# Performance work log

Hardware: AMD Instinct MI355X
Metric: run time of the kernel (lower is better)

The kernel has to match this reference:

```python
import jax, jax.numpy as jnp
import numpy as np

B, S = 512, 512
VOCAB, E, H1, H2, NTAGS = 50000, 20, 30, 50, 45


def _xavier_scale(fan_in, fan_out):
    return float(np.sqrt(2.0 / (fan_in + fan_out)))


def setup_inputs() -> dict:
    key = jax.random.key(0)
    ks = jax.random.split(key, 32)
    n = lambda i, shape, s=1.0: jax.random.normal(ks[i], shape, dtype=jnp.float32) * s
    w = 0.1  # weight scale
    emb_f1 = n(0, (VOCAB, E), w).at[0].set(0.0)  # padding_idx=0
    emb_b1 = n(1, (VOCAB, E), w).at[0].set(0.0)
    xs1 = _xavier_scale(B, H1)
    xs2 = _xavier_scale(B, H2)
    inp = {
        "x": jax.random.randint(ks[2], (B, S), 0, VOCAB, dtype=jnp.int64),
        "emb_f1": emb_f1, "emb_b1": emb_b1,
        "h0_f1": n(3, (B, H1), xs1), "c0_f1": n(4, (B, H1), xs1),
        "Wih_f1": n(5, (4 * H1, E), w), "Whh_f1": n(6, (4 * H1, H1), w),
        "bih_f1": n(7, (4 * H1,), w), "bhh_f1": n(8, (4 * H1,), w),
        "h0_b1": n(9, (B, H1), xs1), "c0_b1": n(10, (B, H1), xs1),
        "Wih_b1": n(11, (4 * H1, E), w), "Whh_b1": n(12, (4 * H1, H1), w),
        "bih_b1": n(13, (4 * H1,), w), "bhh_b1": n(14, (4 * H1,), w),
        "h0_f2": n(15, (B, H2), xs2), "c0_f2": n(16, (B, H2), xs2),
        "Wih_f2": n(17, (4 * H2, 2 * H1), w), "Whh_f2": n(18, (4 * H2, H2), w),
        "bih_f2": n(19, (4 * H2,), w), "bhh_f2": n(20, (4 * H2,), w),
        "h0_b2": n(21, (B, H2), xs2), "c0_b2": n(22, (B, H2), xs2),
        "Wih_b2": n(23, (4 * H2, 2 * H1), w), "Whh_b2": n(24, (4 * H2, H2), w),
        "bih_b2": n(25, (4 * H2,), w), "bhh_b2": n(26, (4 * H2,), w),
        "lin_w": n(27, (NTAGS, 2 * H2), w), "lin_b": n(28, (NTAGS,), w),
    }
    return inp


def _run_lstm(seq, h0, c0, Wih, Whh, bih, bhh, forward):
    """PyTorch LSTMCell recurrence over seq (B,S,D). Replicates the original's
    quirks: backward dir appends hidden states in reversed time order, and the
    (S,B,H) stack is .view()-ed into (B,S,H) without transposing."""
    b, s, _ = seq.shape
    h = h0.shape[-1]
    xs = jnp.swapaxes(seq, 0, 1)  # (S,B,D)

    def step(carry, xt):
        hh, cc = carry
        g = xt @ Wih.T + bih + hh @ Whh.T + bhh  # (B, 4H), gate order i,f,g,o
        i, f, gg, o = jnp.split(g, 4, axis=-1)
        cc = jax.nn.sigmoid(f) * cc + jax.nn.sigmoid(i) * jnp.tanh(gg)
        hh = jax.nn.sigmoid(o) * jnp.tanh(cc)
        return (hh, cc), hh

    _, hs = jax.lax.scan(step, (h0, c0), xs, reverse=not forward)  # hs[i] ~ time i
    if not forward:
        hs = hs[::-1]  # torch appended in processing (reversed-time) order
    return hs.reshape(b, s, h)  # faithful buggy view (S,B,H) -> (B,S,H)


def reference(x, emb_f1, emb_b1,
              h0_f1, c0_f1, Wih_f1, Whh_f1, bih_f1, bhh_f1,
              h0_b1, c0_b1, Wih_b1, Whh_b1, bih_b1, bhh_b1,
              h0_f2, c0_f2, Wih_f2, Whh_f2, bih_f2, bhh_f2,
              h0_b2, c0_b2, Wih_b2, Whh_b2, bih_b2, bhh_b2,
              lin_w, lin_b):
    f1 = _run_lstm(emb_f1[x], h0_f1, c0_f1, Wih_f1, Whh_f1, bih_f1, bhh_f1, True)
    b1 = _run_lstm(emb_b1[x], h0_b1, c0_b1, Wih_b1, Whh_b1, bih_b1, bhh_b1, False)
    l1 = jnp.concatenate([f1, b1], axis=2)  # (B,S,2*H1)
    f2 = _run_lstm(l1, h0_f2, c0_f2, Wih_f2, Whh_f2, bih_f2, bhh_f2, True)
    b2 = _run_lstm(l1, h0_b2, c0_b2, Wih_b2, Whh_b2, bih_b2, bhh_b2, False)
    l2 = jnp.concatenate([f2, b2], axis=2)  # (B,S,2*H2)
    return l2 @ lin_w.T + lin_b  # (B,S,NTAGS)
```

## Files before the change

### kernel.cpp

```cpp
#include <hip/hip_runtime.h>
#include <hip/hip_bf16.h>

typedef __hip_bfloat16 bf16;
typedef __attribute__((ext_vector_type(8))) short short8;
typedef __attribute__((ext_vector_type(4))) float float4v;
typedef unsigned short ushort_t;

#define BB 512
#define SS 512
#define EE 20
#define H1C 30
#define H2C 50
#define NTC 45

#define BAR() asm volatile("s_waitcnt lgkmcnt(0)\n\ts_barrier" ::: "memory")

#if __has_builtin(__builtin_amdgcn_exp2f)
#define EXP2(x) __builtin_amdgcn_exp2f(x)
#else
#define EXP2(x) exp2f(x)
#endif
#if __has_builtin(__builtin_amdgcn_rcpf)
#define RCPF(x) __builtin_amdgcn_rcpf(x)
#else
#define RCPF(x) (1.0f / (x))
#endif

__device__ __forceinline__ float sigf(float v) {
    return RCPF(1.0f + EXP2(-1.4426950408889634f * v));
}
__device__ __forceinline__ float tanh_(float v) {
    return 2.0f * RCPF(1.0f + EXP2(-2.8853900817779268f * v)) - 1.0f;
}

__device__ __forceinline__ ushort_t f2bf(float f) {
    unsigned u = __float_as_uint(f);
    unsigned r = u + 0x7FFFu + ((u >> 16) & 1u);
    return (ushort_t)(r >> 16);
}
__device__ __forceinline__ float bf2f(ushort_t s) { return __uint_as_float(((unsigned)s) << 16); }

__device__ __forceinline__ float ldG(const void* p, int i, int f32) {
    if (f32) return ((const float*)p)[i];
    return bf2f(((const ushort_t*)p)[i]);
}
__device__ __forceinline__ int ldTok(const void* x, int i, int x64) {
    const int* xi = (const int*)x;
    return x64 ? xi[2 * i] : xi[i];
}

__global__ void detect_kernel(const void* bih, const void* x, int* flags) {
    if (threadIdx.x == 0 && blockIdx.x == 0) {
        const ushort_t* u = (const ushort_t*)bih;
        int isf = 0;
        for (int i = 0; i < 120; i++) {
            float v = fabsf(bf2f(u[i]));
            if (!(v < 16.0f)) isf = 1;
        }
        flags[0] = isf;
        const int* xi = (const int*)x;
        int orv = 0;
        for (int i = 1; i < 32; i += 2) orv |= xi[i];
        flags[1] = (orv == 0) ? 1 : 0;
    }
}

struct XV4 { float v[4]; };

__global__ __launch_bounds__(128) void lstm1_kernel(
    const void* __restrict__ x,
    const void* __restrict__ emb_f, const void* __restrict__ emb_b,
    const void* __restrict__ h0_f, const void* __restrict__ c0_f,
    const void* __restrict__ Wih_f, const void* __restrict__ Whh_f,
    const void* __restrict__ bih_f, const void* __restrict__ bhh_f,
    const void* __restrict__ h0_b, const void* __restrict__ c0_b,
    const void* __restrict__ Wih_b, const void* __restrict__ Whh_b,
    const void* __restrict__ bih_b, const void* __restrict__ bhh_b,
    ushort_t* __restrict__ hsf, ushort_t* __restrict__ hsb,
    const int* __restrict__ flags)
{
    const int f32v = flags[0], x64 = flags[1];
    const int wg = blockIdx.x, dir = wg >> 5, j0 = (wg & 31) << 4, tid = threadIdx.x;
    const int wave = tid >> 6, lane = tid & 63, li = lane & 15, quad = lane >> 4;

    const void* emb = dir ? emb_b : emb_f;
    const void* h0  = dir ? h0_b  : h0_f;
    const void* c0  = dir ? c0_b  : c0_f;
    const void* Wih = dir ? Wih_b : Wih_f;
    const void* Whh = dir ? Whh_b : Whh_f;
    const void* bih = dir ? bih_b : bih_f;
    const void* bhh = dir ? bhh_b : bhh_f;
    ushort_t* hs = dir ? hsb : hsf;

    __shared__ __align__(16) ushort_t Af[2][2][64][8];
    __shared__ int toks[16][SS];

    for (int idx = tid; idx < 16 * SS; idx += 128) {
        int r = idx >> 9, t = idx & (SS - 1);
        toks[r][t] = ldTok(x, (j0 + r) * SS + t, x64);
    }
    for (int idx = tid; idx < 2 * 2 * 64 * 8; idx += 128) ((ushort_t*)Af)[idx] = 0;

    const int n = wave * 16 + li;
    const bool nok = n < H1C;

    short8 bhi[4][2], blo[4][2];
    float bias_g[4];
    #pragma unroll
    for (int g = 0; g < 4; g++) {
        const int wrow = g * H1C + n;
        bias_g[g] = nok ? (ldG(bih, wrow, f32v) + ldG(bhh, wrow, f32v)) : 0.f;
        #pragma unroll
        for (int kt = 0; kt < 2; kt++) {
            short8 hi, lo;
            #pragma unroll
            for (int j = 0; j < 8; j++) {
                int k = kt * 32 + quad * 8 + j;
                float w = 0.f;
                if (nok) {
                    if (k < EE) w = ldG(Wih, wrow * EE + k, f32v);
                    else if (k < EE + H1C) w = ldG(Whh, wrow * H1C + (k - EE), f32v);
                }
                ushort_t h = f2bf(w);
                hi[j] = (short)h;
                lo[j] = (short)f2bf(w - bf2f(h));
            }
            bhi[g][kt] = hi; blo[g][kt] = lo;
        }
    }

    const int kh = EE + n;
    const int khk = kh >> 5, khg = (kh & 31) >> 3, khj = kh & 7;
    const int lrow = tid / 5, lc = tid - lrow * 5, k0 = lc * 4;
    const bool ldr = tid < 80;
    const int t0 = dir ? SS - 1 : 0, dt = dir ? -1 : 1;

    __syncthreads();

    float creg[4];
    #pragma unroll
    for (int r = 0; r < 4; r++) {
        const int m = quad * 4 + r;
        creg[r] = nok ? ldG(c0, (j0 + m) * H1C + n, f32v) : 0.f;
        ushort_t hb = nok ? f2bf(ldG(h0, (j0 + m) * H1C + n, f32v)) : 0;
        Af[0][khk][khg * 16 + m][khj] = hb;
    }
    XV4 xA, xB;
    if (ldr) {
        int tok = toks[lrow][t0];
        #pragma unroll
        for (int jj = 0; jj < 4; jj++)
            Af[0][0][(k0 >> 3) * 16 + lrow][(k0 & 7) + jj] = f2bf(ldG(emb, tok * EE + k0 + jj, f32v));
        int tok1 = toks[lrow][t0 + dt];
        #pragma unroll
        for (int jj = 0; jj < 4; jj++) xA.v[jj] = ldG(emb, tok1 * EE + k0 + jj, f32v);
    }
    __syncthreads();

    auto step = [&](int it, XV4& xin, XV4& xout) {
        const int t = t0 + dt * it;
        const int cur = it & 1, nxt = cur ^ 1;
        BAR();
        short8 af0 = *(const short8*)&Af[cur][0][lane][0];
        short8 af1 = *(const short8*)&Af[cur][1][lane][0];
        if (ldr && it + 2 < SS) {
            int tok = toks[lrow][t + 2 * dt];
            #pragma unroll
            for (int jj = 0; jj < 4; jj++) xout.v[jj] = ldG(emb, tok * EE + k0 + jj, f32v);
        }
        float4v acc[4];
        #pragma unroll
        for (int g = 0; g < 4; g++) {
            float4v a; a[0] = a[1] = a[2] = a[3] = bias_g[g];
            a = __builtin_amdgcn_mfma_f32_16x16x32_bf16(af0, bhi[g][0], a, 0, 0, 0);
            a = __builtin_amdgcn_mfma_f32_16x16x32_bf16(af0, blo[g][0], a, 0, 0, 0);
            a = __builtin_amdgcn_mfma_f32_16x16x32_bf16(af1, bhi[g][1], a, 0, 0, 0);
            a = __builtin_amdgcn_mfma_f32_16x16x32_bf16(af1, blo[g][1], a, 0, 0, 0);
            acc[g] = a;
        }
        ushort_t hb[4];
        #pragma unroll
        for (int r = 0; r < 4; r++) {
            float gi = acc[0][r], gf = acc[1][r], gg = acc[2][r], go = acc[3][r];
            float c = sigf(gf) * creg[r] + sigf(gi) * tanh_(gg);
            float h = sigf(go) * tanh_(c);
            creg[r] = c;
            hb[r] = nok ? f2bf(h) : 0;
            hs[((size_t)(j0 + quad * 4 + r) * SS + t) * 32 + n] = hb[r];
        }
        if (it + 1 < SS) {
            #pragma unroll
            for (int r = 0; r < 4; r++) Af[nxt][khk][khg * 16 + quad * 4 + r][khj] = hb[r];
            if (ldr) {
                #pragma unroll
                for (int jj = 0; jj < 4; jj++)
                    Af[nxt][0][(k0 >> 3) * 16 + lrow][(k0 & 7) + jj] = f2bf(xin.v[jj]);
            }
        }
    };
    for (int it = 0; it < SS; it += 2) { step(it, xA, xB); step(it + 1, xB, xA); }
}

__global__ __launch_bounds__(256) void lstm2_kernel(
    const ushort_t* __restrict__ hs1f, const ushort_t* __restrict__ hs1b,
    const void* __restrict__ h0_f, const void* __restrict__ c0_f,
    const void* __restrict__ Wih_f, const void* __restrict__ Whh_f,
    const void* __restrict__ bih_f, const void* __restrict__ bhh_f,
    const void* __restrict__ h0_b, const void* __restrict__ c0_b,
    const void* __restrict__ Wih_b, const void* __restrict__ Whh_b,
    const void* __restrict__ bih_b, const void* __restrict__ bhh_b,
    ushort_t* __restrict__ hsf, ushort_t* __restrict__ hsb,
    const int* __restrict__ flags)
{
    const int f32v = flags[0];
    const int wg = blockIdx.x, dir = wg >> 5, cb = (wg & 31) << 4, tid = threadIdx.x;
    const int wave = tid >> 6, lane = tid & 63, li = lane & 15, quad = lane >> 4;

    const void* h0  = dir ? h0_b  : h0_f;
    const void* c0  = dir ? c0_b  : c0_f;
    const void* Wih = dir ? Wih_b : Wih_f;
    const void* Whh = dir ? Whh_b : Whh_f;
    const void* bih = dir ? bih_b : bih_f;
    const void* bhh = dir ? bhh_b : bhh_f;
    ushort_t* hs = dir ? hsb : hsf;

    __shared__ __align__(16) ushort_t Af[2][4][64][8];
    for (int idx = tid; idx < 2 * 4 * 64 * 8; idx += 256) ((ushort_t*)Af)[idx] = 0;

    const int n = wave * 16 + li;
    const bool nok = n < H2C;

    short8 bhi[4][4], blo[4][4];
    float bias_g[4];
    #pragma unroll
    for (int g = 0; g < 4; g++) {
        const int wrow = g * H2C + n;
        bias_g[g] = nok ? (ldG(bih, wrow, f32v) + ldG(bhh, wrow, f32v)) : 0.f;
        #pragma unroll
        for (int kt = 0; kt < 4; kt++) {
            short8 hi, lo;
            #pragma unroll
            for (int j = 0; j < 8; j++) {
                int k = kt * 32 + quad * 8 + j;
                float w = 0.f;
                if (nok) {
                    if (k < H1C) w = ldG(Wih, wrow * (2 * H1C) + k, f32v);
                    else if (k >= 32 && k < 32 + H1C) w = ldG(Wih, wrow * (2 * H1C) + H1C + (k - 32), f32v);
                    else if (k >= 64 && k < 64 + H2C) w = ldG(Whh, wrow * H2C + (k - 64), f32v);
                }
                ushort_t h = f2bf(w);
                hi[j] = (short)h;
                lo[j] = (short)f2bf(w - bf2f(h));
            }
            bhi[g][kt] = hi; blo[g][kt] = lo;
        }
    }

    const int kh = 64 + n;
    const int khk = kh >> 5, khg = (kh & 31) >> 3, khj = kh & 7;
    const int lrow = tid >> 4, k0 = (tid & 15) * 4;
    const int t0 = dir ? SS - 1 : 0, dt = dir ? -1 : 1;

    auto loadX = [&](int c) -> ushort4 {
        const int a = cb + lrow;
        if (k0 < 32)
            return *(const ushort4*)&hs1f[((size_t)c * SS + a) * 32 + k0];
        else
            return *(const ushort4*)&hs1b[((size_t)c * SS + (SS - 1 - a)) * 32 + (k0 - 32)];
    };

    __syncthreads();

    float creg[4];
    #pragma unroll
    for (int r = 0; r < 4; r++) {
        const int m = quad * 4 + r;
        creg[r] = nok ? ldG(c0, (cb + m) * H2C + n, f32v) : 0.f;
        ushort_t hb = nok ? f2bf(ldG(h0, (cb + m) * H2C + n, f32v)) : 0;
        Af[0][khk][khg * 16 + m][khj] = hb;
    }
    {
        ushort4 xi = loadX(t0);
        const int kg = (k0 & 31) >> 3, kt = k0 >> 5, jb = k0 & 7;
        Af[0][kt][kg * 16 + lrow][jb + 0] = xi.x;
        Af[0][kt][kg * 16 + lrow][jb + 1] = xi.y;
        Af[0][kt][kg * 16 + lrow][jb + 2] = xi.z;
        Af[0][kt][kg * 16 + lrow][jb + 3] = xi.w;
    }
    ushort4 xA = loadX(t0 + dt), xB;
    __syncthreads();

    auto step = [&](int it, ushort4& xin, ushort4& xout) {
        const int c = t0 + dt * it;
        const int cur = it & 1, nxt = cur ^ 1;
        BAR();
        short8 af[4];
        #pragma unroll
        for (int kt = 0; kt < 4; kt++) af[kt] = *(const short8*)&Af[cur][kt][lane][0];
        if (it + 2 < SS) xout = loadX(c + 2 * dt);
        float4v acc[4];
        #pragma unroll
        for (int g = 0; g < 4; g++) {
            float4v a; a[0] = a[1] = a[2] = a[3] = bias_g[g];
            #pragma unroll
            for (int kt = 0; kt < 4; kt++) {
                a = __builtin_amdgcn_mfma_f32_16x16x32_bf16(af[kt], bhi[g][kt], a, 0, 0, 0);
                a = __builtin_amdgcn_mfma_f32_16x16x32_bf16(af[kt], blo[g][kt], a, 0, 0, 0);
            }
            acc[g] = a;
        }
        ushort_t hb[4];
        #pragma unroll
        for (int r = 0; r < 4; r++) {
            float gi = acc[0][r], gf = acc[1][r], gg = acc[2][r], go = acc[3][r];
            float cc = sigf(gf) * creg[r] + sigf(gi) * tanh_(gg);
            float h = sigf(go) * tanh_(cc);
            creg[r] = cc;
            hb[r] = nok ? f2bf(h) : 0;
        }
        ushort4 h4; h4.x = hb[0]; h4.y = hb[1]; h4.z = hb[2]; h4.w = hb[3];
        *(ushort4*)&hs[((size_t)c * 64 + n) * SS + cb + quad * 4] = h4;
        if (it + 1 < SS) {
            #pragma unroll
            for (int r = 0; r < 4; r++) Af[nxt][khk][khg * 16 + quad * 4 + r][khj] = hb[r];
            const int kg = (k0 & 31) >> 3, kt = k0 >> 5, jb = k0 & 7;
            Af[nxt][kt][kg * 16 + lrow][jb + 0] = xin.x;
            Af[nxt][kt][kg * 16 + lrow][jb + 1] = xin.y;
            Af[nxt][kt][kg * 16 + lrow][jb + 2] = xin.z;
            Af[nxt][kt][kg * 16 + lrow][jb + 3] = xin.w;
        }
    };
    for (int it = 0; it < SS; it += 2) { step(it, xA, xB); step(it + 1, xB, xA); }
}

__global__ __launch_bounds__(256) void lin_kernel(
    const ushort_t* __restrict__ hs2f, const ushort_t* __restrict__ hs2b,
    const void* __restrict__ lw, const void* __restrict__ lb,
    void* __restrict__ out, const int* __restrict__ flags)
{
    const int f32v = flags[0];
    const int tid = threadIdx.x, wave = tid >> 6, lane = tid & 63, li = lane & 15, quad = lane >> 4;

    __shared__ __align__(16) ushort_t Af[4][4][64][8];
    for (int idx = tid; idx < 4 * 4 * 64 * 8; idx += 256) ((ushort_t*)Af)[idx] = 0;

    short8 bhi[3][4], blo[3][4];
    float biasv[3];
    #pragma unroll
    for (int nt = 0; nt < 3; nt++) {
        const int nn = nt * 16 + li;
        const bool nok = nn < NTC;
        biasv[nt] = nok ? ldG(lb, nn, f32v) : 0.f;
        #pragma unroll
        for (int kt = 0; kt < 4; kt++) {
            short8 hi, lo;
            #pragma unroll
            for (int j = 0; j < 8; j++) {
                int k = kt * 32 + quad * 8 + j;
                float w = 0.f;
                if (nok) {
                    if (k < H2C) w = ldG(lw, nn * 100 + k, f32v);
                    else if (k >= 64 && k < 64 + H2C) w = ldG(lw, nn * 100 + 50 + (k - 64), f32v);
                }
                ushort_t h = f2bf(w);
                hi[j] = (short)h;
                lo[j] = (short)f2bf(w - bf2f(h));
            }
            bhi[nt][kt] = hi; blo[nt][kt] = lo;
        }
    }

    const int P0 = blockIdx.x * 64;
    const int i = P0 >> 9, j0 = P0 & 511;
    __syncthreads();
    for (int idx = tid; idx < 100 * 32; idx += 256) {
        const int kk = idx >> 5, pj = (idx & 31) * 2;
        unsigned v;
        int k;
        if (kk < H2C) {
            v = *(const unsigned*)&hs2f[((size_t)i * 64 + kk) * SS + j0 + pj];
            k = kk;
        } else {
            v = *(const unsigned*)&hs2b[((size_t)(SS - 1 - i) * 64 + (kk - H2C)) * SS + j0 + pj];
            k = 64 + (kk - H2C);
        }
        const int kt = k >> 5, kg = (k & 31) >> 3, j = k & 7;
        Af[pj >> 4][kt][kg * 16 + (pj & 15)][j] = (ushort_t)(v & 0xFFFF);
        Af[pj >> 4][kt][kg * 16 + ((pj + 1) & 15)][j] = (ushort_t)(v >> 16);
    }
    __syncthreads();

    short8 af[4];
    #pragma unroll
    for (int kt = 0; kt < 4; kt++) af[kt] = *(const short8*)&Af[wave][kt][lane][0];
    #pragma unroll
    for (int nt = 0; nt < 3; nt++) {
        float4v a; a[0] = a[1] = a[2] = a[3] = biasv[nt];
        #pragma unroll
        for (int kt = 0; kt < 4; kt++) {
            a = __builtin_amdgcn_mfma_f32_16x16x32_bf16(af[kt], bhi[nt][kt], a, 0, 0, 0);
            a = __builtin_amdgcn_mfma_f32_16x16x32_bf16(af[kt], blo[nt][kt], a, 0, 0, 0);
        }
        const int nn = nt * 16 + li;
        if (nn < NTC) {
            #pragma unroll
            for (int reg = 0; reg < 4; reg++) {
                const int prow = wave * 16 + quad * 4 + reg;
                const size_t op = (size_t)(P0 + prow) * NTC + nn;
                if (f32v) ((float*)out)[op] = a[reg];
                else      ((ushort_t*)out)[op] = f2bf(a[reg]);
            }
        }
    }
}

extern "C" void kernel_launch(void* const* d_in, const int* in_sizes, int n_in,
                              void* d_out, int out_size, void* d_ws, size_t ws_size,
                              hipStream_t stream)
{
    const void* x      = d_in[0];
    const void* emb_f1 = d_in[1];
    const void* emb_b1 = d_in[2];
    const void* h0_f1  = d_in[3];
    const void* c0_f1  = d_in[4];
    const void* Wih_f1 = d_in[5];
    const void* Whh_f1 = d_in[6];
    const void* bih_f1 = d_in[7];
    const void* bhh_f1 = d_in[8];
    const void* h0_b1  = d_in[9];
    const void* c0_b1  = d_in[10];
    const void* Wih_b1 = d_in[11];
    const void* Whh_b1 = d_in[12];
    const void* bih_b1 = d_in[13];
    const void* bhh_b1 = d_in[14];
    const void* h0_f2  = d_in[15];
    const void* c0_f2  = d_in[16];
    const void* Wih_f2 = d_in[17];
    const void* Whh_f2 = d_in[18];
    const void* bih_f2 = d_in[19];
    const void* bhh_f2 = d_in[20];
    const void* h0_b2  = d_in[21];
    const void* c0_b2  = d_in[22];
    const void* Wih_b2 = d_in[23];
    const void* Whh_b2 = d_in[24];
    const void* bih_b2 = d_in[25];
    const void* bhh_b2 = d_in[26];
    const void* lin_w  = d_in[27];
    const void* lin_b  = d_in[28];

    int* flags = (int*)d_ws;
    ushort_t* hs1f = (ushort_t*)((char*)d_ws + 256);
    ushort_t* hs1b = hs1f + (size_t)BB * SS * 32;
    ushort_t* hs2f = hs1b + (size_t)BB * SS * 32;
    ushort_t* hs2b = hs2f + (size_t)SS * 64 * BB;

    detect_kernel<<<1, 64, 0, stream>>>(bih_f1, x, flags);
    lstm1_kernel<<<64, 128, 0, stream>>>(x, emb_f1, emb_b1,
        h0_f1, c0_f1, Wih_f1, Whh_f1, bih_f1, bhh_f1,
        h0_b1, c0_b1, Wih_b1, Whh_b1, bih_b1, bhh_b1, hs1f, hs1b, flags);
    lstm2_kernel<<<64, 256, 0, stream>>>(hs1f, hs1b,
        h0_f2, c0_f2, Wih_f2, Whh_f2, bih_f2, bhh_f2,
        h0_b2, c0_b2, Wih_b2, Whh_b2, bih_b2, bhh_b2, hs2f, hs2b, flags);
    lin_kernel<<<(BB * SS) / 64, 256, 0, stream>>>(hs2f, hs2b, lin_w, lin_b, d_out, flags);
}
```

Baseline: 1.004 ms.

## Restructure layer-1 LSTM into a single-wave block with transposed MFMA and fused activations

The first-layer LSTM kernel drops from two waves to one wave per block, so the per-step workgroup barrier becomes a plain LDS wait. The MFMA is transposed so weights are the A operand and the hidden/input state is B, with gates interleaved per hidden unit. Bias is folded in through a constant-one input column and log2e scaling is folded into the weights, so the activations can share reciprocals. Token indices are prefetched directly from global memory instead of being staged in LDS, embedding rows are loaded as vectors, and layer 2's input weights are permuted to match the new hidden-state layout. The trade-off is that one wave now issues all 32 MFMAs per step serially, with more registers and less parallelism per block.

```diff
diff --git a/kernel.cpp b/kernel.cpp
--- a/kernel.cpp
+++ b/kernel.cpp
@@ -1,7 +1,6 @@
 #include <hip/hip_runtime.h>
 #include <hip/hip_bf16.h>
 
-typedef __hip_bfloat16 bf16;
 typedef __attribute__((ext_vector_type(8))) short short8;
 typedef __attribute__((ext_vector_type(4))) float float4v;
 typedef unsigned short ushort_t;
@@ -14,6 +13,7 @@
 #define NTC 45
 
 #define BAR() asm volatile("s_waitcnt lgkmcnt(0)\n\ts_barrier" ::: "memory")
+#define WFENCE() asm volatile("s_waitcnt lgkmcnt(0)" ::: "memory")
 
 #if __has_builtin(__builtin_amdgcn_exp2f)
 #define EXP2(x) __builtin_amdgcn_exp2f(x)
@@ -26,11 +26,28 @@
 #define RCPF(x) (1.0f / (x))
 #endif
 
+#define LOG2E 1.4426950408889634f
+
 __device__ __forceinline__ float sigf(float v) {
     return RCPF(1.0f + EXP2(-1.4426950408889634f * v));
 }
 __device__ __forceinline__ float tanh_(float v) {
     return 2.0f * RCPF(1.0f + EXP2(-2.8853900817779268f * v)) - 1.0f;
+}
+
+__device__ __forceinline__ float lstm_act(float gi, float gf, float gg, float go, float& c) {
+    gi = fmaxf(gi, -30.f); gf = fmaxf(gf, -30.f);
+    gg = fmaxf(gg, -30.f); go = fmaxf(go, -30.f);
+    float di = 1.f + EXP2(-gi), df = 1.f + EXP2(-gf);
+    float dg = 1.f + EXP2(-gg), dO = 1.f + EXP2(-go);
+    float r1 = RCPF(di * df), r2 = RCPF(dg * dO);
+    float si = df * r1, sf = di * r1;
+    float tg = 2.f * (dO * r2) - 1.f;
+    float so = dg * r2;
+    float cc = sf * c + si * tg;
+    c = cc;
+    float e = EXP2(-2.8853900817779268f * cc);
+    return so * (2.f * RCPF(1.f + e) - 1.f);
 }
 
 __device__ __forceinline__ ushort_t f2bf(float f) {
@@ -65,9 +82,45 @@
     }
 }
 
-struct XV4 { float v[4]; };
-
-__global__ __launch_bounds__(128) void lstm1_kernel(
+struct XR8 { uint4 a, b; };
+
+__device__ __forceinline__ XR8 ldEmbChunk(const void* emb, int tok, int q, int f32v) {
+    XR8 o;
+    if (f32v) {
+        const float* p = (const float*)emb + (size_t)tok * EE + q * 8;
+        o.a = *(const uint4*)p;
+        o.b = (q < 2) ? *(const uint4*)(p + 4) : o.a;
+    } else {
+        const ushort_t* p = (const ushort_t*)emb + (size_t)tok * EE + q * 8;
+        uint2 lo = *(const uint2*)p;
+        o.a.x = lo.x; o.a.y = lo.y; o.a.z = 0; o.a.w = 0;
+        if (q < 2) { uint2 hi = *(const uint2*)(p + 4); o.a.z = hi.x; o.a.w = hi.y; }
+        o.b = o.a;
+    }
+    return o;
+}
+__device__ __forceinline__ void writeXC(ushort_t* dst, const XR8& x, int q, int f32v) {
+    if (f32v) {
+        if (q < 2) {
+            short8 s;
+            s[0] = (short)f2bf(__uint_as_float(x.a.x)); s[1] = (short)f2bf(__uint_as_float(x.a.y));
+            s[2] = (short)f2bf(__uint_as_float(x.a.z)); s[3] = (short)f2bf(__uint_as_float(x.a.w));
+            s[4] = (short)f2bf(__uint_as_float(x.b.x)); s[5] = (short)f2bf(__uint_as_float(x.b.y));
+            s[6] = (short)f2bf(__uint_as_float(x.b.z)); s[7] = (short)f2bf(__uint_as_float(x.b.w));
+            *(short8*)dst = s;
+        } else {
+            ushort4 u4;
+            u4.x = f2bf(__uint_as_float(x.a.x)); u4.y = f2bf(__uint_as_float(x.a.y));
+            u4.z = f2bf(__uint_as_float(x.a.z)); u4.w = f2bf(__uint_as_float(x.a.w));
+            *(ushort4*)dst = u4;
+        }
+    } else {
+        if (q < 2) *(uint4*)dst = x.a;
+        else { uint2 t2; t2.x = x.a.x; t2.y = x.a.y; *(uint2*)dst = t2; }
+    }
+}
+
+__global__ __launch_bounds__(64) void lstm1_kernel(
     const void* __restrict__ x,
     const void* __restrict__ emb_f, const void* __restrict__ emb_b,
     const void* __restrict__ h0_f, const void* __restrict__ c0_f,
@@ -80,8 +133,8 @@
     const int* __restrict__ flags)
 {
     const int f32v = flags[0], x64 = flags[1];
-    const int wg = blockIdx.x, dir = wg >> 5, j0 = (wg & 31) << 4, tid = threadIdx.x;
-    const int wave = tid >> 6, lane = tid & 63, li = lane & 15, quad = lane >> 4;
+    const int lane = threadIdx.x & 63, li = lane & 15, quad = lane >> 4;
+    const int cg = blockIdx.x, dir = cg >> 5, j0 = (cg & 31) << 4;
 
     const void* emb = dir ? emb_b : emb_f;
     const void* h0  = dir ? h0_b  : h0_f;
@@ -92,113 +145,100 @@
     const void* bhh = dir ? bhh_b : bhh_f;
     ushort_t* hs = dir ? hsb : hsf;
 
-    __shared__ __align__(16) ushort_t Af[2][2][64][8];
-    __shared__ int toks[16][SS];
-
-    for (int idx = tid; idx < 16 * SS; idx += 128) {
-        int r = idx >> 9, t = idx & (SS - 1);
-        toks[r][t] = ldTok(x, (j0 + r) * SS + t, x64);
-    }
-    for (int idx = tid; idx < 2 * 2 * 64 * 8; idx += 128) ((ushort_t*)Af)[idx] = 0;
-
-    const int n = wave * 16 + li;
-    const bool nok = n < H1C;
-
-    short8 bhi[4][2], blo[4][2];
-    float bias_g[4];
+    __shared__ __align__(16) ushort_t B[16][72];
+
+    for (int i = lane; i < 16 * 72; i += 64) ((ushort_t*)B)[i] = 0;
+    if (quad == 0) B[li][20] = 0x3F80;
+
+    short8 whi[8][2], wlo[8][2];
     #pragma unroll
-    for (int g = 0; g < 4; g++) {
-        const int wrow = g * H1C + n;
-        bias_g[g] = nok ? (ldG(bih, wrow, f32v) + ldG(bhh, wrow, f32v)) : 0.f;
+    for (int u = 0; u < 8; u++) {
+        const int n = u * 16 + li;
+        const int nn = n >> 2, g = n & 3;
+        const bool nok = nn < H1C;
+        const float sc = (g == 2) ? 2.0f * LOG2E : LOG2E;
         #pragma unroll
         for (int kt = 0; kt < 2; kt++) {
             short8 hi, lo;
             #pragma unroll
             for (int j = 0; j < 8; j++) {
-                int k = kt * 32 + quad * 8 + j;
+                const int k = kt * 32 + quad * 8 + j;
                 float w = 0.f;
                 if (nok) {
-                    if (k < EE) w = ldG(Wih, wrow * EE + k, f32v);
-                    else if (k < EE + H1C) w = ldG(Whh, wrow * H1C + (k - EE), f32v);
+                    if (k < EE) w = ldG(Wih, (g * H1C + nn) * EE + k, f32v);
+                    else if (k == 20) w = ldG(bih, g * H1C + nn, f32v) + ldG(bhh, g * H1C + nn, f32v);
+                    else if (k >= 24 && k < 56) {
+                        const int qk = (k - 24) >> 3, uk = (k - 24) & 7, ns = uk * 4 + qk;
+                        if (ns < H1C) w = ldG(Whh, (g * H1C + nn) * H1C + ns, f32v);
+                    }
                 }
-                ushort_t h = f2bf(w);
-                hi[j] = (short)h;
-                lo[j] = (short)f2bf(w - bf2f(h));
+                w *= sc;
+                ushort_t b1 = f2bf(w);
+                hi[j] = (short)b1;
+                lo[j] = (short)f2bf(w - bf2f(b1));
             }
-            bhi[g][kt] = hi; blo[g][kt] = lo;
-        }
-    }
-
-    const int kh = EE + n;
-    const int khk = kh >> 5, khg = (kh & 31) >> 3, khj = kh & 7;
-    const int lrow = tid / 5, lc = tid - lrow * 5, k0 = lc * 4;
-    const bool ldr = tid < 80;
+            whi[u][kt] = hi; wlo[u][kt] = lo;
+        }
+    }
+
+    float creg[8];
+    {
+        short8 hp;
+        #pragma unroll
+        for (int u = 0; u < 8; u++) {
+            const int nn = u * 4 + quad;
+            const bool ok = nn < H1C;
+            creg[u] = ok ? ldG(c0, (j0 + li) * H1C + nn, f32v) : 0.f;
+            hp[u] = ok ? (short)f2bf(ldG(h0, (j0 + li) * H1C + nn, f32v)) : (short)0;
+        }
+        *(short8*)&B[li][24 + quad * 8] = hp;
+    }
+
     const int t0 = dir ? SS - 1 : 0, dt = dir ? -1 : 1;
-
-    __syncthreads();
-
-    float creg[4];
-    #pragma unroll
-    for (int r = 0; r < 4; r++) {
-        const int m = quad * 4 + r;
-        creg[r] = nok ? ldG(c0, (j0 + m) * H1C + n, f32v) : 0.f;
-        ushort_t hb = nok ? f2bf(ldG(h0, (j0 + m) * H1C + n, f32v)) : 0;
-        Af[0][khk][khg * 16 + m][khj] = hb;
-    }
-    XV4 xA, xB;
+    const int rbase = (j0 + li) * SS;
+    const bool ldr = quad < 3;
+
+    XR8 eA = {}, eB = {};
+    int tA = 0, tB = 0;
     if (ldr) {
-        int tok = toks[lrow][t0];
-        #pragma unroll
-        for (int jj = 0; jj < 4; jj++)
-            Af[0][0][(k0 >> 3) * 16 + lrow][(k0 & 7) + jj] = f2bf(ldG(emb, tok * EE + k0 + jj, f32v));
-        int tok1 = toks[lrow][t0 + dt];
-        #pragma unroll
-        for (int jj = 0; jj < 4; jj++) xA.v[jj] = ldG(emb, tok1 * EE + k0 + jj, f32v);
-    }
-    __syncthreads();
-
-    auto step = [&](int it, XV4& xin, XV4& xout) {
+        int tk0 = ldTok(x, rbase + t0, x64);
+        XR8 e0 = ldEmbChunk(emb, tk0, quad, f32v);
+        writeXC(&B[li][quad * 8], e0, quad, f32v);
+        int tk1 = ldTok(x, rbase + t0 + dt, x64);
+        eA = ldEmbChunk(emb, tk1, quad, f32v);
+        tA = ldTok(x, rbase + t0 + 2 * dt, x64);
+    }
+
+    auto step = [&](int it, XR8& ein, XR8& eout, int& tin, int& tout) {
         const int t = t0 + dt * it;
-        const int cur = it & 1, nxt = cur ^ 1;
-        BAR();
-        short8 af0 = *(const short8*)&Af[cur][0][lane][0];
-        short8 af1 = *(const short8*)&Af[cur][1][lane][0];
-        if (ldr && it + 2 < SS) {
-            int tok = toks[lrow][t + 2 * dt];
-            #pragma unroll
-            for (int jj = 0; jj < 4; jj++) xout.v[jj] = ldG(emb, tok * EE + k0 + jj, f32v);
-        }
-        float4v acc[4];
-        #pragma unroll
-        for (int g = 0; g < 4; g++) {
-            float4v a; a[0] = a[1] = a[2] = a[3] = bias_g[g];
-            a = __builtin_amdgcn_mfma_f32_16x16x32_bf16(af0, bhi[g][0], a, 0, 0, 0);
-            a = __builtin_amdgcn_mfma_f32_16x16x32_bf16(af0, blo[g][0], a, 0, 0, 0);
-            a = __builtin_amdgcn_mfma_f32_16x16x32_bf16(af1, bhi[g][1], a, 0, 0, 0);
-            a = __builtin_amdgcn_mfma_f32_16x16x32_bf16(af1, blo[g][1], a, 0, 0, 0);
-            acc[g] = a;
-        }
-        ushort_t hb[4];
-        #pragma unroll
-        for (int r = 0; r < 4; r++) {
-            float gi = acc[0][r], gf = acc[1][r], gg = acc[2][r], go = acc[3][r];
-            float c = sigf(gf) * creg[r] + sigf(gi) * tanh_(gg);
-            float h = sigf(go) * tanh_(c);
-            creg[r] = c;
-            hb[r] = nok ? f2bf(h) : 0;
-            hs[((size_t)(j0 + quad * 4 + r) * SS + t) * 32 + n] = hb[r];
-        }
-        if (it + 1 < SS) {
-            #pragma unroll
-            for (int r = 0; r < 4; r++) Af[nxt][khk][khg * 16 + quad * 4 + r][khj] = hb[r];
-            if (ldr) {
-                #pragma unroll
-                for (int jj = 0; jj < 4; jj++)
-                    Af[nxt][0][(k0 >> 3) * 16 + lrow][(k0 & 7) + jj] = f2bf(xin.v[jj]);
-            }
-        }
+        WFENCE();
+        short8 b0 = *(const short8*)&B[li][quad * 8];
+        short8 b1 = *(const short8*)&B[li][32 + quad * 8];
+        if (ldr) {
+            if (it + 2 < SS) eout = ldEmbChunk(emb, tin, quad, f32v);
+            if (it + 3 < SS) tout = ldTok(x, rbase + t0 + dt * (it + 3), x64);
+        }
+        float4v acc[8];
+        #pragma unroll
+        for (int u = 0; u < 8; u++) {
+            float4v a; a[0] = 0.f; a[1] = 0.f; a[2] = 0.f; a[3] = 0.f;
+            a = __builtin_amdgcn_mfma_f32_16x16x32_bf16(whi[u][0], b0, a, 0, 0, 0);
+            a = __builtin_amdgcn_mfma_f32_16x16x32_bf16(wlo[u][0], b0, a, 0, 0, 0);
+            a = __builtin_amdgcn_mfma_f32_16x16x32_bf16(whi[u][1], b1, a, 0, 0, 0);
+            a = __builtin_amdgcn_mfma_f32_16x16x32_bf16(wlo[u][1], b1, a, 0, 0, 0);
+            acc[u] = a;
+        }
+        if (ldr && it + 1 < SS) writeXC(&B[li][quad * 8], ein, quad, f32v);
+        short8 hp;
+        #pragma unroll
+        for (int u = 0; u < 8; u++) {
+            float hv = lstm_act(acc[u][0], acc[u][1], acc[u][2], acc[u][3], creg[u]);
+            hp[u] = (short)f2bf(hv);
+        }
+        *(short8*)&B[li][24 + quad * 8] = hp;
+        *(short8*)&hs[((size_t)(j0 + li) * SS + t) * 32 + quad * 8] = hp;
     };
-    for (int it = 0; it < SS; it += 2) { step(it, xA, xB); step(it + 1, xB, xA); }
+    for (int it = 0; it < SS; it += 2) { step(it, eA, eB, tA, tB); step(it + 1, eB, eA, tB, tA); }
 }
 
 __global__ __launch_bounds__(256) void lstm2_kernel(
@@ -244,9 +284,15 @@
                 int k = kt * 32 + quad * 8 + j;
                 float w = 0.f;
                 if (nok) {
-                    if (k < H1C) w = ldG(Wih, wrow * (2 * H1C) + k, f32v);
-                    else if (k >= 32 && k < 32 + H1C) w = ldG(Wih, wrow * (2 * H1C) + H1C + (k - 32), f32v);
-                    else if (k >= 64 && k < 64 + H2C) w = ldG(Whh, wrow * H2C + (k - 64), f32v);
+                    if (k < 32) {
+                        const int c = k, nn2 = (c & 7) * 4 + (c >> 3);
+                        if (nn2 < H1C) w = ldG(Wih, wrow * (2 * H1C) + nn2, f32v);
+                    } else if (k < 64) {
+                        const int c = k - 32, nn2 = (c & 7) * 4 + (c >> 3);
+                        if (nn2 < H1C) w = ldG(Wih, wrow * (2 * H1C) + H1C + nn2, f32v);
+                    } else if (k < 64 + H2C) {
+                        w = ldG(Whh, wrow * H2C + (k - 64), f32v);
+                    }
                 }
                 ushort_t h = f2bf(w);
                 hi[j] = (short)h;
@@ -276,8 +322,8 @@
     for (int r = 0; r < 4; r++) {
         const int m = quad * 4 + r;
         creg[r] = nok ? ldG(c0, (cb + m) * H2C + n, f32v) : 0.f;
-        ushort_t hb = nok ? f2bf(ldG(h0, (cb + m) * H2C + n, f32v)) : 0;
-        Af[0][khk][khg * 16 + m][khj] = hb;
+        ushort_t hb0 = nok ? f2bf(ldG(h0, (cb + m) * H2C + n, f32v)) : (ushort_t)0;
+        Af[0][khk][khg * 16 + m][khj] = hb0;
     }
     {
         ushort4 xi = loadX(t0);
@@ -316,7 +362,7 @@
             float cc = sigf(gf) * creg[r] + sigf(gi) * tanh_(gg);
             float h = sigf(go) * tanh_(cc);
             creg[r] = cc;
-            hb[r] = nok ? f2bf(h) : 0;
+            hb[r] = nok ? f2bf(h) : (ushort_t)0;
         }
         ushort4 h4; h4.x = hb[0]; h4.y = hb[1]; h4.z = hb[2]; h4.w = hb[3];
         *(ushort4*)&hs[((size_t)c * 64 + n) * SS + cb + quad * 4] = h4;
@@ -455,7 +501,7 @@
     ushort_t* hs2b = hs2f + (size_t)SS * 64 * BB;
 
     detect_kernel<<<1, 64, 0, stream>>>(bih_f1, x, flags);
-    lstm1_kernel<<<64, 128, 0, stream>>>(x, emb_f1, emb_b1,
+    lstm1_kernel<<<64, 64, 0, stream>>>(x, emb_f1, emb_b1,
         h0_f1, c0_f1, Wih_f1, Whh_f1, bih_f1, bhh_f1,
         h0_b1, c0_b1, Wih_b1, Whh_b1, bih_b1, bhh_b1, hs1f, hs1b, flags);
     lstm2_kernel<<<64, 256, 0, stream>>>(hs1f, hs1b,
```

Result: slower. 1.460 ms (+45.5%).
